# Kernel optimization log

Measured on AMD Instinct MI355X. Metric: run time of the kernel, lower is better.

## Reference

```python
import jax, jax.numpy as jnp
import numpy as np

B, S, D, H, F = 8, 1024, 1024, 16, 4096
DH = D // H  # 64
EPS = 1e-12


def _layer_norm(x, g, b):
    mu = jnp.mean(x, axis=-1, keepdims=True)
    var = jnp.mean(jnp.square(x - mu), axis=-1, keepdims=True)
    return (x - mu) / jnp.sqrt(var + EPS) * g + b


def setup_inputs() -> dict:
    key = jax.random.key(0)
    ks = jax.random.split(key, 16)
    sd = 0.02
    inp = {
        "x": jax.random.normal(ks[0], (B, S, D), dtype=jnp.float32),
        "attn_mask": jnp.ones((B, S), dtype=jnp.int32),
        # attention projections (torch Linear: W is [out, in])
        "Wq": jax.random.normal(ks[1], (D, D), dtype=jnp.float32) * sd,
        "bq": jnp.zeros((D,), dtype=jnp.float32),
        "Wk": jax.random.normal(ks[2], (D, D), dtype=jnp.float32) * sd,
        "bk": jnp.zeros((D,), dtype=jnp.float32),
        "Wv": jax.random.normal(ks[3], (D, D), dtype=jnp.float32) * sd,
        "bv": jnp.zeros((D,), dtype=jnp.float32),
        "Wo": jax.random.normal(ks[4], (D, D), dtype=jnp.float32) * sd,
        "bo": jnp.zeros((D,), dtype=jnp.float32),
        # sa_layer_norm
        "ln1_g": jnp.ones((D,), dtype=jnp.float32),
        "ln1_b": jnp.zeros((D,), dtype=jnp.float32),
        # FFN
        "W1": jax.random.normal(ks[5], (F, D), dtype=jnp.float32) * sd,
        "b1": jnp.zeros((F,), dtype=jnp.float32),
        "W2": jax.random.normal(ks[6], (D, F), dtype=jnp.float32) * sd,
        "b2": jnp.zeros((D,), dtype=jnp.float32),
        # output_layer_norm
        "ln2_g": jnp.ones((D,), dtype=jnp.float32),
        "ln2_b": jnp.zeros((D,), dtype=jnp.float32),
    }
    return inp


def reference(x, attn_mask, Wq, bq, Wk, bk, Wv, bv, Wo, bo,
              ln1_g, ln1_b, W1, b1, W2, b2, ln2_g, ln2_b):
    b, s, d = x.shape

    def proj_heads(inp, W, bias):
        y = jnp.einsum('bsd,ed->bse', inp, W) + bias  # torch Linear: x @ W.T + b
        return y.reshape(b, s, H, DH).transpose(0, 2, 1, 3)  # (b, h, s, dh)

    q = proj_heads(x, Wq, bq) / jnp.sqrt(jnp.float32(DH))
    k = proj_heads(x, Wk, bk)
    v = proj_heads(x, Wv, bv)

    scores = jnp.einsum('bhqe,bhke->bhqk', q, k)  # (b, h, s, s)
    pad = (attn_mask == 0)[:, None, None, :]      # (b, 1, 1, s)
    scores = jnp.where(pad, -jnp.inf, scores)
    weights = jax.nn.softmax(scores, axis=-1)

    ctx = jnp.einsum('bhqk,bhke->bhqe', weights, v)
    ctx = ctx.transpose(0, 2, 1, 3).reshape(b, s, d)
    sa_out = jnp.einsum('bsd,ed->bse', ctx, Wo) + bo

    h = _layer_norm(sa_out + x, ln1_g, ln1_b)

    ff = jnp.einsum('bsd,fd->bsf', h, W1) + b1
    ff = jax.nn.gelu(ff, approximate=False)
    ff = jnp.einsum('bsf,df->bsd', ff, W2) + b2

    out = _layer_norm(ff + h, ln2_g, ln2_b)
    return out
```

## Files before the change

kernel.cpp:

```cpp
#include <hip/hip_runtime.h>
#include <math.h>

typedef __attribute__((ext_vector_type(8))) short short8;
typedef __attribute__((ext_vector_type(4))) float f32x4;

__device__ __forceinline__ unsigned short f2bf(float f) {
  unsigned int u = __float_as_uint(f);
  u += 0x7fffu + ((u >> 16) & 1u);
  return (unsigned short)(u >> 16);
}

__device__ __forceinline__ void gll16(const unsigned short* g, unsigned short* l) {
  __builtin_amdgcn_global_load_lds(
      (const __attribute__((address_space(1))) unsigned int*)(uintptr_t)g,
      (__attribute__((address_space(3))) unsigned int*)(uintptr_t)l, 16, 0, 0);
}

__global__ __launch_bounds__(256) void cvt_f32_bf16(const float* __restrict__ in,
                                                    unsigned short* __restrict__ out,
                                                    int n4) {
  int i = blockIdx.x * 256 + threadIdx.x;
  if (i >= n4) return;
  float4 f = reinterpret_cast<const float4*>(in)[i];
  ushort4 o;
  o.x = f2bf(f.x); o.y = f2bf(f.y); o.z = f2bf(f.z); o.w = f2bf(f.w);
  reinterpret_cast<ushort4*>(out)[i] = o;
}

__global__ __launch_bounds__(256) void cvt4_f32_bf16(
    const float* __restrict__ a, const float* __restrict__ b,
    const float* __restrict__ c, const float* __restrict__ d,
    unsigned short* __restrict__ oa, unsigned short* __restrict__ ob,
    unsigned short* __restrict__ oc, unsigned short* __restrict__ od) {
  const float* in = (blockIdx.y == 0) ? a : (blockIdx.y == 1) ? b : (blockIdx.y == 2) ? c : d;
  unsigned short* out = (blockIdx.y == 0) ? oa : (blockIdx.y == 1) ? ob : (blockIdx.y == 2) ? oc : od;
  int i = blockIdx.x * 256 + threadIdx.x;
  float4 f = reinterpret_cast<const float4*>(in)[i];
  ushort4 o;
  o.x = f2bf(f.x); o.y = f2bf(f.y); o.z = f2bf(f.z); o.w = f2bf(f.w);
  reinterpret_cast<ushort4*>(out)[i] = o;
}

template <int EPI>
__global__ __launch_bounds__(256) void gemm_nt(
    const unsigned short* __restrict__ A, const unsigned short* __restrict__ B,
    const float* __restrict__ bias, const float* __restrict__ bias_k,
    const float* __restrict__ bias_v, int K, int N, float scale,
    const float* __restrict__ resid, unsigned short* __restrict__ outb,
    float* __restrict__ outf) {
  __shared__ __align__(16) unsigned short As[128 * 32];
  __shared__ __align__(16) unsigned short Bs[128 * 32];
  const int t = threadIdx.x;
  const int tm = blockIdx.y * 128, tn = blockIdx.x * 128;
  const int lane = t & 63, wv = t >> 6;
  const int wr = wv >> 1, wc = wv & 1;
  const int l15 = lane & 15, quad = lane >> 4;
  const int srow = lane >> 2;
  const int scol = (lane & 3) << 3;

  const f32x4 zero = {0.f, 0.f, 0.f, 0.f};
  f32x4 acc[4][4];
#pragma unroll
  for (int i = 0; i < 4; ++i)
#pragma unroll
    for (int j = 0; j < 4; ++j) acc[i][j] = zero;

  for (int k0 = 0; k0 < K; k0 += 32) {
    __syncthreads();
#pragma unroll
    for (int i = 0; i < 2; ++i) {
      const int seg = wv * 2 + i;
      const int r = seg * 16 + srow;
      gll16(&A[(size_t)(tm + r) * K + k0 + scol], &As[seg * 512]);
      gll16(&B[(size_t)(tn + r) * K + k0 + scol], &Bs[seg * 512]);
    }
    __syncthreads();
    short8 af[4], bfr[4];
#pragma unroll
    for (int i = 0; i < 4; ++i) {
      af[i] = *reinterpret_cast<const short8*>(&As[(wr * 64 + i * 16 + l15) * 32 + quad * 8]);
      bfr[i] = *reinterpret_cast<const short8*>(&Bs[(wc * 64 + i * 16 + l15) * 32 + quad * 8]);
    }
#pragma unroll
    for (int i = 0; i < 4; ++i)
#pragma unroll
      for (int j = 0; j < 4; ++j)
        acc[i][j] = __builtin_amdgcn_mfma_f32_16x16x32_bf16(af[i], bfr[j], acc[i][j], 0, 0, 0);
  }

  if (EPI == 5) {
    const int chunk = tn >> 10;
    const float* bp = (chunk == 0) ? bias : (chunk == 1) ? bias_k : bias_v;
    const float sc = (chunk == 0) ? 0.125f : 1.f;
#pragma unroll
    for (int i = 0; i < 4; ++i) {
#pragma unroll
      for (int j = 0; j < 4; ++j) {
        const int colc = (tn & 1023) + wc * 64 + j * 16 + l15;
        const float bcol = bp[colc];
        const int h = colc >> 6, dh = colc & 63;
        const int row0 = tm + wr * 64 + i * 16 + quad * 4;
        const int b = row0 >> 10, s0 = row0 & 1023;
        if (chunk == 2) {
          ushort4 pk;
          pk.x = f2bf(acc[i][j][0] + bcol);
          pk.y = f2bf(acc[i][j][1] + bcol);
          pk.z = f2bf(acc[i][j][2] + bcol);
          pk.w = f2bf(acc[i][j][3] + bcol);
          *reinterpret_cast<ushort4*>(
              &outb[((size_t)2 << 23) + (((size_t)((b << 4) + h)) << 16) + (dh << 10) + s0]) = pk;
        } else {
#pragma unroll
          for (int r = 0; r < 4; ++r)
            outb[((size_t)chunk << 23) + (((size_t)((b << 4) + h)) << 16) + ((s0 + r) << 6) + dh] =
                f2bf((acc[i][j][r] + bcol) * sc);
        }
      }
    }
  } else {
#pragma unroll
    for (int i = 0; i < 4; ++i) {
#pragma unroll
      for (int j = 0; j < 4; ++j) {
        const int col = tn + wc * 64 + j * 16 + l15;
        const float bcol = bias[col];
        const int row0 = tm + wr * 64 + i * 16 + quad * 4;
#pragma unroll
        for (int r = 0; r < 4; ++r) {
          const int row = row0 + r;
          float v = acc[i][j][r] + bcol;
          if (EPI == 2) {
            float g = 0.5f * v * (1.f + erff(v * 0.70710678118f));
            outb[(size_t)row * (size_t)N + col] = f2bf(g);
          } else {
            size_t idx = (size_t)row * (size_t)N + col;
            outf[idx] = v + resid[idx];
          }
        }
      }
    }
  }
}

__global__ __launch_bounds__(256) void attn_kernel(
    const unsigned short* __restrict__ Q, const unsigned short* __restrict__ Kc,
    const unsigned short* __restrict__ Vg, const int* __restrict__ mask,
    unsigned short* __restrict__ ctx) {
  __shared__ __align__(16) unsigned short Qs[64 * 64];
  __shared__ __align__(16) unsigned short Ks[64 * 64];
  __shared__ __align__(16) unsigned short Vs[64 * 64];
  __shared__ __align__(16) unsigned short Ps[4 * 16 * 72];
  __shared__ float maskf[1024];
  const int t = threadIdx.x;
  const int bh = blockIdx.x;
  const int qt = blockIdx.y;
  const int b = bh >> 4, h = bh & 15;
  const int lane = t & 63, wv = t >> 6, l15 = lane & 15, quad = lane >> 4;
  const int lr = lane >> 3;
  const int cs = (lane & 7) ^ lr;
  const unsigned short* Qp = Q + ((size_t)bh << 16);
  const unsigned short* Kp = Kc + ((size_t)bh << 16);
  const unsigned short* Vp = Vg + ((size_t)bh << 16);

  for (int i = t; i < 1024; i += 256)
    maskf[i] = mask[b * 1024 + i] ? -8.f : -INFINITY;
#pragma unroll
  for (int i = 0; i < 2; ++i) {
    const int seg = wv * 2 + i;
    gll16(&Qp[(qt * 64 + seg * 8 + lr) * 64 + cs * 8], &Qs[seg * 512]);
  }
  __syncthreads();
  const int sw0 = ((quad ^ (l15 & 7)) << 3);
  const int sw1 = (((quad + 4) ^ (l15 & 7)) << 3);
  const short8 qf0 = *reinterpret_cast<const short8*>(&Qs[(wv * 16 + l15) * 64 + sw0]);
  const short8 qf1 = *reinterpret_cast<const short8*>(&Qs[(wv * 16 + l15) * 64 + sw1]);

  const f32x4 zero = {0.f, 0.f, 0.f, 0.f};
  float ps[4] = {0.f, 0.f, 0.f, 0.f};
  f32x4 o[4];
#pragma unroll
  for (int j = 0; j < 4; ++j) o[j] = zero;

  unsigned short* Pw = &Ps[wv * 16 * 72];
  for (int kt = 0; kt < 16; ++kt) {
    __syncthreads();
#pragma unroll
    for (int i = 0; i < 2; ++i) {
      const int seg = wv * 2 + i;
      const int row = seg * 8 + lr;
      gll16(&Kp[(kt * 64 + row) * 64 + cs * 8], &Ks[seg * 512]);
      gll16(&Vp[row * 1024 + kt * 64 + cs * 8], &Vs[seg * 512]);
    }
    __syncthreads();

    f32x4 s4[4];
    float madd[4];
#pragma unroll
    for (int nt = 0; nt < 4; ++nt) {
      const int row = nt * 16 + l15;
      short8 kf0 = *reinterpret_cast<const short8*>(&Ks[row * 64 + sw0]);
      short8 kf1 = *reinterpret_cast<const short8*>(&Ks[row * 64 + sw1]);
      s4[nt] = __builtin_amdgcn_mfma_f32_16x16x32_bf16(qf0, kf0, zero, 0, 0, 0);
      s4[nt] = __builtin_amdgcn_mfma_f32_16x16x32_bf16(qf1, kf1, s4[nt], 0, 0, 0);
      madd[nt] = maskf[kt * 64 + nt * 16 + l15];
    }
#pragma unroll
    for (int nt = 0; nt < 4; ++nt) {
#pragma unroll
      for (int r = 0; r < 4; ++r) {
        float p = __expf(s4[nt][r] + madd[nt]);
        ps[r] += p;
        Pw[(quad * 4 + r) * 72 + nt * 16 + l15] = f2bf(p);
      }
    }
    short8 pf0 = *reinterpret_cast<const short8*>(&Pw[l15 * 72 + quad * 8]);
    short8 pf1 = *reinterpret_cast<const short8*>(&Pw[l15 * 72 + 32 + quad * 8]);
#pragma unroll
    for (int nt = 0; nt < 4; ++nt) {
      const int row = nt * 16 + l15;
      short8 vf0 = *reinterpret_cast<const short8*>(&Vs[row * 64 + sw0]);
      short8 vf1 = *reinterpret_cast<const short8*>(&Vs[row * 64 + sw1]);
      o[nt] = __builtin_amdgcn_mfma_f32_16x16x32_bf16(pf0, vf0, o[nt], 0, 0, 0);
      o[nt] = __builtin_amdgcn_mfma_f32_16x16x32_bf16(pf1, vf1, o[nt], 0, 0, 0);
    }
  }

#pragma unroll
  for (int r = 0; r < 4; ++r) {
#pragma unroll
    for (int off = 8; off >= 1; off >>= 1) ps[r] += __shfl_xor(ps[r], off, 64);
  }
#pragma unroll
  for (int r = 0; r < 4; ++r) {
    float inv = 1.f / ps[r];
    int srow = qt * 64 + wv * 16 + quad * 4 + r;
#pragma unroll
    for (int nt = 0; nt < 4; ++nt) {
      int dh = nt * 16 + l15;
      ctx[((size_t)b << 20) + ((size_t)srow << 10) + (h << 6) + dh] = f2bf(o[nt][r] * inv);
    }
  }
}

__global__ __launch_bounds__(256) void ln_kernel(float* __restrict__ y,
                                                 const float* __restrict__ g,
                                                 const float* __restrict__ be,
                                                 unsigned short* __restrict__ hb) {
  __shared__ float sm[8];
  const int t = threadIdx.x;
  const size_t row = blockIdx.x;
  float* yr = y + (row << 10);
  float v[4];
#pragma unroll
  for (int i = 0; i < 4; ++i) v[i] = yr[t + (i << 8)];
  float s = v[0] + v[1] + v[2] + v[3];
#pragma unroll
  for (int off = 32; off >= 1; off >>= 1) s += __shfl_xor(s, off, 64);
  if ((t & 63) == 0) sm[t >> 6] = s;
  __syncthreads();
  float mu = (sm[0] + sm[1] + sm[2] + sm[3]) * (1.f / 1024.f);
  float q = 0.f;
#pragma unroll
  for (int i = 0; i < 4; ++i) { float d = v[i] - mu; q += d * d; }
#pragma unroll
  for (int off = 32; off >= 1; off >>= 1) q += __shfl_xor(q, off, 64);
  if ((t & 63) == 0) sm[4 + (t >> 6)] = q;
  __syncthreads();
  float var = (sm[4] + sm[5] + sm[6] + sm[7]) * (1.f / 1024.f);
  float rs = rsqrtf(var + 1e-12f);
#pragma unroll
  for (int i = 0; i < 4; ++i) {
    int c = t + (i << 8);
    float o = (v[i] - mu) * rs * g[c] + be[c];
    yr[c] = o;
    if (hb) hb[(row << 10) + c] = f2bf(o);
  }
}

extern "C" void kernel_launch(void* const* d_in, const int* in_sizes, int n_in,
                              void* d_out, int out_size, void* d_ws, size_t ws_size,
                              hipStream_t stream) {
  const float* x   = (const float*)d_in[0];
  const int*   msk = (const int*)d_in[1];
  const float* Wq  = (const float*)d_in[2];
  const float* bq  = (const float*)d_in[3];
  const float* Wk  = (const float*)d_in[4];
  const float* bk  = (const float*)d_in[5];
  const float* Wv  = (const float*)d_in[6];
  const float* bv  = (const float*)d_in[7];
  const float* Wo  = (const float*)d_in[8];
  const float* bo  = (const float*)d_in[9];
  const float* g1  = (const float*)d_in[10];
  const float* be1 = (const float*)d_in[11];
  const float* W1  = (const float*)d_in[12];
  const float* b1  = (const float*)d_in[13];
  const float* W2  = (const float*)d_in[14];
  const float* b2  = (const float*)d_in[15];
  const float* g2  = (const float*)d_in[16];
  const float* be2 = (const float*)d_in[17];
  float* out = (float*)d_out;

  unsigned short* Wqb = (unsigned short*)d_ws;
  unsigned short* Wkb = Wqb + (1u << 20);
  unsigned short* Wvb = Wkb + (1u << 20);
  unsigned short* Wob = Wvb + (1u << 20);
  unsigned short* W1b = Wob + (1u << 20);
  unsigned short* W2b = W1b + (4u << 20);
  unsigned short* xb  = W2b + (4u << 20);
  unsigned short* qb  = xb + (8u << 20);
  unsigned short* vb  = qb + (16u << 20);
  unsigned short* ctx = xb;
  unsigned short* ffb = xb;
  float* y1 = (float*)(qb + (24u << 20));
  unsigned short* hb = (unsigned short*)(y1 + (8u << 20));

  dim3 blk(256);
  cvt4_f32_bf16<<<dim3(1024, 4), blk, 0, stream>>>(Wq, Wk, Wv, Wo, Wqb, Wkb, Wvb, Wob);
  cvt_f32_bf16<<<dim3(4096), blk, 0, stream>>>(W1, W1b, 1 << 20);
  cvt_f32_bf16<<<dim3(4096), blk, 0, stream>>>(W2, W2b, 1 << 20);
  cvt_f32_bf16<<<dim3(8192), blk, 0, stream>>>(x, xb, 1 << 21);
  gemm_nt<5><<<dim3(24, 64), blk, 0, stream>>>(xb, Wqb, bq, bk, bv, 1024, 1024, 1.f,
                                               nullptr, qb, nullptr);
  attn_kernel<<<dim3(128, 16), blk, 0, stream>>>(qb, qb + (8u << 20), vb, msk, ctx);
  gemm_nt<1><<<dim3(8, 64), blk, 0, stream>>>(ctx, Wob, bo, nullptr, nullptr, 1024, 1024,
                                              1.f, x, nullptr, y1);
  ln_kernel<<<dim3(8192), blk, 0, stream>>>(y1, g1, be1, hb);
  gemm_nt<2><<<dim3(32, 64), blk, 0, stream>>>(hb, W1b, b1, nullptr, nullptr, 1024, 4096,
                                               1.f, nullptr, ffb, nullptr);
  gemm_nt<1><<<dim3(8, 64), blk, 0, stream>>>(ffb, W2b, b2, nullptr, nullptr, 4096, 1024,
                                              1.f, y1, nullptr, out);
  ln_kernel<<<dim3(8192), blk, 0, stream>>>(out, g2, be2, nullptr);
}
```

Before: 590.6 us.

## Swap MFMA operands for vectorized epilogues, swizzle tiles, fast GELU, split V GEMM

Adds a SWAP mode that exchanges MFMA operands so each lane holds four consecutive output columns. Bias, residual and output stores in the epilogues then become float4/ushort4 vector accesses instead of scalar strided ones. The V projection moves to its own non-swapped GEMM that writes the transposed layout. Other changes: a grouped block-index swizzle for L2 reuse, precomputed load pointers, and an Abramowitz-Stegun erf approximation in place of erff for GELU. The erf approximation slightly changes numerical accuracy, and the extra launch adds overhead.

```diff
diff --git a/kernel.cpp b/kernel.cpp
--- a/kernel.cpp
+++ b/kernel.cpp
@@ -8,6 +8,17 @@
   unsigned int u = __float_as_uint(f);
   u += 0x7fffu + ((u >> 16) & 1u);
   return (unsigned short)(u >> 16);
+}
+
+__device__ __forceinline__ float gelu_f(float v) {
+  float xa = fabsf(v) * 0.70710678118f;
+  float t = __builtin_amdgcn_rcpf(1.f + 0.3275911f * xa);
+  float p = t * (0.254829592f +
+            t * (-0.284496736f +
+            t * (1.421413741f +
+            t * (-1.453152027f + t * 1.061405429f))));
+  float erfa = 1.f - p * __expf(-xa * xa);
+  return 0.5f * v * (1.f + copysignf(erfa, v));
 }
 
 __device__ __forceinline__ void gll16(const unsigned short* g, unsigned short* l) {
@@ -41,23 +52,34 @@
   reinterpret_cast<ushort4*>(out)[i] = o;
 }
 
-template <int EPI>
+template <int EPI, bool SWAP>
 __global__ __launch_bounds__(256) void gemm_nt(
     const unsigned short* __restrict__ A, const unsigned short* __restrict__ B,
     const float* __restrict__ bias, const float* __restrict__ bias_k,
-    const float* __restrict__ bias_v, int K, int N, float scale,
-    const float* __restrict__ resid, unsigned short* __restrict__ outb,
-    float* __restrict__ outf) {
+    int K, int N, const float* __restrict__ resid,
+    unsigned short* __restrict__ outb, float* __restrict__ outf) {
   __shared__ __align__(16) unsigned short As[128 * 32];
   __shared__ __align__(16) unsigned short Bs[128 * 32];
   const int t = threadIdx.x;
-  const int tm = blockIdx.y * 128, tn = blockIdx.x * 128;
+  const int lin = blockIdx.x + gridDim.x * blockIdx.y;
+  const int rem = lin & (gridDim.x * 8 - 1);
+  const int mt = (lin / (gridDim.x * 8)) * 8 + (rem & 7);
+  const int tm = mt * 128, tn = (rem >> 3) * 128;
   const int lane = t & 63, wv = t >> 6;
   const int wr = wv >> 1, wc = wv & 1;
   const int l15 = lane & 15, quad = lane >> 4;
   const int srow = lane >> 2;
   const int scol = (lane & 3) << 3;
 
+  const unsigned short* pa0 = &A[(size_t)(tm + (wv * 2) * 16 + srow) * K + scol];
+  const unsigned short* pa1 = &A[(size_t)(tm + (wv * 2 + 1) * 16 + srow) * K + scol];
+  const unsigned short* pb0 = &B[(size_t)(tn + (wv * 2) * 16 + srow) * K + scol];
+  const unsigned short* pb1 = &B[(size_t)(tn + (wv * 2 + 1) * 16 + srow) * K + scol];
+  unsigned short* la0 = &As[(wv * 2) * 512];
+  unsigned short* la1 = &As[(wv * 2 + 1) * 512];
+  unsigned short* lb0 = &Bs[(wv * 2) * 512];
+  unsigned short* lb1 = &Bs[(wv * 2 + 1) * 512];
+
   const f32x4 zero = {0.f, 0.f, 0.f, 0.f};
   f32x4 acc[4][4];
 #pragma unroll
@@ -67,13 +89,10 @@
 
   for (int k0 = 0; k0 < K; k0 += 32) {
     __syncthreads();
-#pragma unroll
-    for (int i = 0; i < 2; ++i) {
-      const int seg = wv * 2 + i;
-      const int r = seg * 16 + srow;
-      gll16(&A[(size_t)(tm + r) * K + k0 + scol], &As[seg * 512]);
-      gll16(&B[(size_t)(tn + r) * K + k0 + scol], &Bs[seg * 512]);
-    }
+    gll16(pa0, la0); pa0 += 32;
+    gll16(pa1, la1); pa1 += 32;
+    gll16(pb0, lb0); pb0 += 32;
+    gll16(pb1, lb1); pb1 += 32;
     __syncthreads();
     short8 af[4], bfr[4];
 #pragma unroll
@@ -85,35 +104,51 @@
     for (int i = 0; i < 4; ++i)
 #pragma unroll
       for (int j = 0; j < 4; ++j)
-        acc[i][j] = __builtin_amdgcn_mfma_f32_16x16x32_bf16(af[i], bfr[j], acc[i][j], 0, 0, 0);
-  }
-
-  if (EPI == 5) {
-    const int chunk = tn >> 10;
-    const float* bp = (chunk == 0) ? bias : (chunk == 1) ? bias_k : bias_v;
-    const float sc = (chunk == 0) ? 0.125f : 1.f;
+        acc[i][j] = SWAP
+            ? __builtin_amdgcn_mfma_f32_16x16x32_bf16(bfr[j], af[i], acc[i][j], 0, 0, 0)
+            : __builtin_amdgcn_mfma_f32_16x16x32_bf16(af[i], bfr[j], acc[i][j], 0, 0, 0);
+  }
+
+  if (SWAP) {
 #pragma unroll
     for (int i = 0; i < 4; ++i) {
+      const int row = tm + wr * 64 + i * 16 + l15;
 #pragma unroll
       for (int j = 0; j < 4; ++j) {
-        const int colc = (tn & 1023) + wc * 64 + j * 16 + l15;
-        const float bcol = bp[colc];
-        const int h = colc >> 6, dh = colc & 63;
-        const int row0 = tm + wr * 64 + i * 16 + quad * 4;
-        const int b = row0 >> 10, s0 = row0 & 1023;
-        if (chunk == 2) {
+        const int col0 = tn + wc * 64 + j * 16 + quad * 4;
+        if (EPI == 5) {
+          const int chunk = col0 >> 10;
+          const int colc = col0 & 1023;
+          const float4 b4 = *reinterpret_cast<const float4*>(
+              &(chunk == 0 ? bias : bias_k)[colc]);
+          const float sc = (chunk == 0) ? 0.125f : 1.f;
+          const int h = colc >> 6, dh = colc & 63;
+          const int b = row >> 10, s = row & 1023;
           ushort4 pk;
-          pk.x = f2bf(acc[i][j][0] + bcol);
-          pk.y = f2bf(acc[i][j][1] + bcol);
-          pk.z = f2bf(acc[i][j][2] + bcol);
-          pk.w = f2bf(acc[i][j][3] + bcol);
+          pk.x = f2bf((acc[i][j][0] + b4.x) * sc);
+          pk.y = f2bf((acc[i][j][1] + b4.y) * sc);
+          pk.z = f2bf((acc[i][j][2] + b4.z) * sc);
+          pk.w = f2bf((acc[i][j][3] + b4.w) * sc);
           *reinterpret_cast<ushort4*>(
-              &outb[((size_t)2 << 23) + (((size_t)((b << 4) + h)) << 16) + (dh << 10) + s0]) = pk;
+              &outb[((size_t)chunk << 23) + (((size_t)((b << 4) + h)) << 16) + (s << 6) + dh]) = pk;
+        } else if (EPI == 2) {
+          const float4 b4 = *reinterpret_cast<const float4*>(&bias[col0]);
+          ushort4 pk;
+          pk.x = f2bf(gelu_f(acc[i][j][0] + b4.x));
+          pk.y = f2bf(gelu_f(acc[i][j][1] + b4.y));
+          pk.z = f2bf(gelu_f(acc[i][j][2] + b4.z));
+          pk.w = f2bf(gelu_f(acc[i][j][3] + b4.w));
+          *reinterpret_cast<ushort4*>(&outb[(size_t)row * (size_t)N + col0]) = pk;
         } else {
-#pragma unroll
-          for (int r = 0; r < 4; ++r)
-            outb[((size_t)chunk << 23) + (((size_t)((b << 4) + h)) << 16) + ((s0 + r) << 6) + dh] =
-                f2bf((acc[i][j][r] + bcol) * sc);
+          const float4 b4 = *reinterpret_cast<const float4*>(&bias[col0]);
+          const size_t idx = (size_t)row * (size_t)N + col0;
+          const float4 r4 = *reinterpret_cast<const float4*>(&resid[idx]);
+          float4 o4;
+          o4.x = acc[i][j][0] + b4.x + r4.x;
+          o4.y = acc[i][j][1] + b4.y + r4.y;
+          o4.z = acc[i][j][2] + b4.z + r4.z;
+          o4.w = acc[i][j][3] + b4.w + r4.w;
+          *reinterpret_cast<float4*>(&outf[idx]) = o4;
         }
       }
     }
@@ -124,19 +159,16 @@
       for (int j = 0; j < 4; ++j) {
         const int col = tn + wc * 64 + j * 16 + l15;
         const float bcol = bias[col];
+        const int h = col >> 6, dh = col & 63;
         const int row0 = tm + wr * 64 + i * 16 + quad * 4;
-#pragma unroll
-        for (int r = 0; r < 4; ++r) {
-          const int row = row0 + r;
-          float v = acc[i][j][r] + bcol;
-          if (EPI == 2) {
-            float g = 0.5f * v * (1.f + erff(v * 0.70710678118f));
-            outb[(size_t)row * (size_t)N + col] = f2bf(g);
-          } else {
-            size_t idx = (size_t)row * (size_t)N + col;
-            outf[idx] = v + resid[idx];
-          }
-        }
+        const int b = row0 >> 10, s0 = row0 & 1023;
+        ushort4 pk;
+        pk.x = f2bf(acc[i][j][0] + bcol);
+        pk.y = f2bf(acc[i][j][1] + bcol);
+        pk.z = f2bf(acc[i][j][2] + bcol);
+        pk.w = f2bf(acc[i][j][3] + bcol);
+        *reinterpret_cast<ushort4*>(
+            &outb[(((size_t)((b << 4) + h)) << 16) + (dh << 10) + s0]) = pk;
       }
     }
   }
@@ -319,15 +351,17 @@
   cvt_f32_bf16<<<dim3(4096), blk, 0, stream>>>(W1, W1b, 1 << 20);
   cvt_f32_bf16<<<dim3(4096), blk, 0, stream>>>(W2, W2b, 1 << 20);
   cvt_f32_bf16<<<dim3(8192), blk, 0, stream>>>(x, xb, 1 << 21);
-  gemm_nt<5><<<dim3(24, 64), blk, 0, stream>>>(xb, Wqb, bq, bk, bv, 1024, 1024, 1.f,
-                                               nullptr, qb, nullptr);
+  gemm_nt<5, true><<<dim3(16, 64), blk, 0, stream>>>(xb, Wqb, bq, bk, 1024, 1024,
+                                                     nullptr, qb, nullptr);
+  gemm_nt<4, false><<<dim3(8, 64), blk, 0, stream>>>(xb, Wvb, bv, nullptr, 1024, 1024,
+                                                     nullptr, vb, nullptr);
   attn_kernel<<<dim3(128, 16), blk, 0, stream>>>(qb, qb + (8u << 20), vb, msk, ctx);
-  gemm_nt<1><<<dim3(8, 64), blk, 0, stream>>>(ctx, Wob, bo, nullptr, nullptr, 1024, 1024,
-                                              1.f, x, nullptr, y1);
+  gemm_nt<1, true><<<dim3(8, 64), blk, 0, stream>>>(ctx, Wob, bo, nullptr, 1024, 1024,
+                                                    x, nullptr, y1);
   ln_kernel<<<dim3(8192), blk, 0, stream>>>(y1, g1, be1, hb);
-  gemm_nt<2><<<dim3(32, 64), blk, 0, stream>>>(hb, W1b, b1, nullptr, nullptr, 1024, 4096,
-                                               1.f, nullptr, ffb, nullptr);
-  gemm_nt<1><<<dim3(8, 64), blk, 0, stream>>>(ffb, W2b, b2, nullptr, nullptr, 4096, 1024,
-                                              1.f, y1, nullptr, out);
+  gemm_nt<2, true><<<dim3(32, 64), blk, 0, stream>>>(hb, W1b, b1, nullptr, 1024, 4096,
+                                                     nullptr, ffb, nullptr);
+  gemm_nt<1, true><<<dim3(8, 64), blk, 0, stream>>>(ffb, W2b, b2, nullptr, 4096, 1024,
+                                                    y1, nullptr, out);
   ln_kernel<<<dim3(8192), blk, 0, stream>>>(out, g2, be2, nullptr);
 }
```

New measurement: 590.8 us. Within noise of the previous version (+0.0%).
